# Performance work log

Measured on AMD Instinct MI355X. Metric: run time of the kernel, lower is better.

## Reference

```python
import jax, jax.numpy as jnp
import numpy as np

HEAD_SIZE = 128


def setup_inputs() -> dict:
    key = jax.random.key(0)
    k0, k1, k2, k3 = jax.random.split(key, 4)
    B, S, E, H = 4, 4096, 1024, HEAD_SIZE
    x = jax.random.normal(k0, (B, S, E), dtype=jnp.float32)
    scale = 1.0 / np.sqrt(E).astype(np.float32)
    Wq = jax.random.normal(k1, (E, H), dtype=jnp.float32) * scale
    Wk = jax.random.normal(k2, (E, H), dtype=jnp.float32) * scale
    Wv = jax.random.normal(k3, (E, H), dtype=jnp.float32) * scale
    k_mask = jnp.ones((B, S), dtype=jnp.int32)
    return {"x": x, "Wq": Wq, "Wk": Wk, "Wv": Wv, "k_mask": k_mask}


def reference(x, Wq, Wk, Wv, k_mask):
    # Self-attention path (kv=None), causal=True
    Q = x @ Wq  # [B, S, H]
    K = x @ Wk  # [B, S, H]
    V = x @ Wv  # [B, S, H]
    inv_sqrt_h = np.float32(1.0 / np.sqrt(HEAD_SIZE))
    att = jnp.einsum('bqh,bkh->bqk', Q, K) * inv_sqrt_h  # [B, S, S]
    neg_inf = jnp.float32(-jnp.inf)
    # padding mask over keys: [B, 1, S_k]
    att = jnp.where(k_mask[:, None, :] == 0, neg_inf, att)
    # causal mask: tril over (q_len, k_len)
    S = Q.shape[1]
    c_mask = jnp.tril(jnp.ones((S, S), dtype=bool))  # [S, S]
    att = jnp.where(c_mask[None, :, :], att, neg_inf)
    att = jax.nn.softmax(att, axis=-1)
    return att @ V  # [B, S, H]
```

## Files before the change

### kernel.cpp

```cpp
#include <hip/hip_runtime.h>
#include <hip/hip_bf16.h>

typedef unsigned short u16;
typedef __attribute__((ext_vector_type(8))) short bf16x8;
typedef __attribute__((ext_vector_type(4))) float f32x4;
typedef __attribute__((ext_vector_type(4))) unsigned short u16x4;

#define SQ 4096
#define HQ 128
#define NCHUNK 80

__device__ __forceinline__ u16 f2b(float f) {
  unsigned int u = __float_as_uint(f);
  unsigned int r = (u + 0x7fffu + ((u >> 16) & 1u)) >> 16;
  return (u16)r;
}

__device__ __forceinline__ u16 f2b_fast(float f) {
  __hip_bfloat16 h = __float2bfloat16(f);
  return __builtin_bit_cast(u16, h);
}

__device__ __forceinline__ void gload_lds16(const u16* gsrc, u16* ldst) {
  __builtin_amdgcn_global_load_lds((const __attribute__((address_space(1))) void*)gsrc,
                                   (__attribute__((address_space(3))) void*)ldst, 16, 0, 0);
}

__global__ __launch_bounds__(256) void k_wt(const float* __restrict__ Wq, const float* __restrict__ Wk,
                                            const float* __restrict__ Wv, u16* __restrict__ wt) {
  int idx = blockIdx.x * 256 + threadIdx.x;
  int z = idx >> 17, r = idx & 131071, n = r >> 10, k = r & 1023;
  const float* W = (z == 0) ? Wq : (z == 1) ? Wk : Wv;
  wt[idx] = f2b(W[k * 128 + n]);
}

__global__ __launch_bounds__(512, 4) void k_proj(const float* __restrict__ x, const u16* __restrict__ wt,
                                                 u16* __restrict__ qb, u16* __restrict__ kb,
                                                 u16* __restrict__ vt) {
  int blk = blockIdx.x;
  int t = threadIdx.x;
  int w = t >> 6, lane = t & 63;
  int wm = w >> 2, wn = w & 3;
  int lr = lane & 15, lg = lane >> 4;

  __shared__ __align__(16) u16 xl[2][64 * 32];
  __shared__ __align__(16) u16 wl[2][384 * 32];

  int srow = t >> 3, sc8 = t & 7;
  const float* xg = x + (long)(blk * 64 + srow) * 1024 + sc8 * 4;
  int xch = ((sc8 >> 1) ^ ((srow >> 1) & 3));
  int xoff = srow * 32 + xch * 8 + (sc8 & 1) * 4;

  f32x4 acc[2][6];
#pragma unroll
  for (int i = 0; i < 2; ++i)
#pragma unroll
    for (int j = 0; j < 6; ++j) acc[i][j] = (f32x4){0.f, 0.f, 0.f, 0.f};

  auto stage_w = [&](int bufi, int k0) {
#pragma unroll
    for (int i = 0; i < 3; ++i) {
      int ci = i * 512 + t;
      int row = ci >> 2, ch = ci & 3;
      gload_lds16(wt + (long)row * 1024 + k0 + ((ch ^ ((row >> 1) & 3)) << 3),
                  &wl[bufi][0] + ci * 8);
    }
  };

  {
    float4 xa = *(const float4*)(xg);
    stage_w(0, 0);
    u16x4 o;
    o[0] = f2b(xa.x); o[1] = f2b(xa.y); o[2] = f2b(xa.z); o[3] = f2b(xa.w);
    *(u16x4*)(&xl[0][0] + xoff) = o;
  }
  __syncthreads();

  int arow0 = wm * 32 + lr;
  for (int ks = 0; ks < 32; ++ks) {
    int cur = ks & 1;
    float4 xa;
    bool more = (ks + 1 < 32);
    if (more) {
      xa = *(const float4*)(xg + (ks + 1) * 32);
      stage_w(cur ^ 1, (ks + 1) * 32);
    }
    bf16x8 af[2], bf[6];
#pragma unroll
    for (int i = 0; i < 2; ++i) {
      int row = arow0 + i * 16;
      af[i] = *(const bf16x8*)(&xl[cur][0] + row * 32 + ((lg ^ ((row >> 1) & 3)) << 3));
    }
#pragma unroll
    for (int j = 0; j < 6; ++j) {
      int row = wn * 96 + j * 16 + lr;
      bf[j] = *(const bf16x8*)(&wl[cur][0] + row * 32 + ((lg ^ ((row >> 1) & 3)) << 3));
    }
#pragma unroll
    for (int i = 0; i < 2; ++i)
#pragma unroll
      for (int j = 0; j < 6; ++j)
        acc[i][j] = __builtin_amdgcn_mfma_f32_16x16x32_bf16(af[i], bf[j], acc[i][j], 0, 0, 0);
    if (more) {
      u16x4 o;
      o[0] = f2b(xa.x); o[1] = f2b(xa.y); o[2] = f2b(xa.z); o[3] = f2b(xa.w);
      *(u16x4*)(&xl[cur ^ 1][0] + xoff) = o;
    }
    __syncthreads();
  }

#pragma unroll
  for (int i = 0; i < 2; ++i)
#pragma unroll
    for (int j = 0; j < 6; ++j)
#pragma unroll
      for (int r = 0; r < 4; ++r) {
        int m = blk * 64 + wm * 32 + i * 16 + lg * 4 + r;
        int col = wn * 96 + j * 16 + lr;
        int z = col >> 7, cz = col & 127;
        u16 v = f2b(acc[i][j][r]);
        if (z == 0) qb[(long)m * 128 + cz] = v;
        else if (z == 1) kb[(long)m * 128 + cz] = v;
        else { int bb = m >> 12, sR = m & 4095; vt[(long)bb * 524288 + (long)cz * 4096 + sR] = v; }
      }
}

__global__ __launch_bounds__(512, 4) void k_attn(const u16* __restrict__ qb, const u16* __restrict__ kb,
                                                 const u16* __restrict__ vt, const int* __restrict__ kmask,
                                                 float* __restrict__ po, float* __restrict__ pl) {
  const float SCALE_LOG2 = 0.08838834764831845f * 1.4426950408889634f;
  const float MFIX = 24.0f;
  int f = (NCHUNK - 1) - (int)blockIdx.x;
  int b = blockIdx.y;
  int gg = 0;
  while (gg < 3 && f >= 4 * (gg + 1) * (gg + 2)) ++gg;
  int off = f - 4 * gg * (gg + 1);
  int qt2 = 8 * gg + off / (gg + 1);
  int kc = off - (off / (gg + 1)) * (gg + 1);
  int kt0 = kc * 16;
  int kt1 = min(kt0 + 16, 2 * qt2 + 2);

  int t = threadIdx.x, w = t >> 6, lane = t & 63;
  int lr = lane & 15, lg = lane >> 4, sw = lr & 7;
  int qrow0 = qt2 * 128 + w * 16;
  const u16* Q = qb + ((long)(b * SQ + qrow0)) * HQ;
  const u16* K = kb + (long)b * SQ * HQ;
  const u16* V = vt + (long)b * HQ * SQ;
  const int* msk = kmask + b * SQ;

  __shared__ __align__(16) u16 Kl[2][64 * 128];
  __shared__ __align__(16) u16 Vl[2][128 * 64];
  __shared__ __align__(16) u16 plds[8][16 * 64];

  bf16x8 aq[4];
#pragma unroll
  for (int c = 0; c < 4; ++c) aq[c] = *(const bf16x8*)(Q + lr * HQ + c * 32 + lg * 8);

  bf16x8 ones;
#pragma unroll
  for (int e = 0; e < 8; ++e) ones[e] = (short)0x3F80;

  f32x4 o[8];
#pragma unroll
  for (int n = 0; n < 8; ++n) o[n] = (f32x4){0.f, 0.f, 0.f, 0.f};
  f32x4 l_acc = (f32x4){0.f, 0.f, 0.f, 0.f};

  auto stage = [&](int bufi, int kb0) {
    const u16* Kg = K + (long)kb0 * HQ;
    const u16* Vg = V + kb0;
#pragma unroll
    for (int i = 0; i < 2; ++i) {
      int ci = w * 2 + i;
      int o16 = ci * 64 + lane;
      int row = o16 >> 4, ch = o16 & 15;
      gload_lds16(Kg + row * HQ + ((ch ^ (row & 7)) << 3), &Kl[bufi][ci * 512]);
    }
#pragma unroll
    for (int i = 0; i < 2; ++i) {
      int ci = 16 + w * 2 + i;
      int o16 = (ci - 16) * 64 + lane;
      int row = o16 >> 3, ch = o16 & 7;
      gload_lds16(Vg + (long)row * SQ + ((ch ^ (row & 7)) << 3), &Vl[bufi][(ci - 16) * 512]);
    }
  };

  stage(0, kt0 * 64);
  __syncthreads();

  u16* pw = &plds[w][0];
  for (int kt = kt0; kt < kt1; ++kt) {
    int cur = (kt - kt0) & 1;
    int kb0 = kt * 64;
    if (kt + 1 < kt1) stage(cur ^ 1, kb0 + 64);

    if (kb0 <= qrow0 + 15) {
      f32x4 s[4];
#pragma unroll
      for (int h = 0; h < 4; ++h) {
        f32x4 acc = (f32x4){0.f, 0.f, 0.f, 0.f};
        const u16* Kp = &Kl[cur][(h * 16 + lr) * 128];
#pragma unroll
        for (int c = 0; c < 4; ++c) {
          bf16x8 bk = *(const bf16x8*)(Kp + (((c * 4 + lg) ^ sw) << 3));
          acc = __builtin_amdgcn_mfma_f32_16x16x32_bf16(aq[c], bk, acc, 0, 0, 0);
        }
        s[h] = acc;
      }
      float mf[4];
#pragma unroll
      for (int h = 0; h < 4; ++h) mf[h] = (msk[kb0 + h * 16 + lr] != 0) ? 1.0f : 0.0f;
      bool needc = (kb0 + 63 > qrow0);
#pragma unroll
      for (int r = 0; r < 4; ++r) {
        int row = lg * 4 + r;
        int qr = qrow0 + row;
#pragma unroll
        for (int h = 0; h < 4; ++h) {
          float p = __builtin_exp2f(fmaf(s[h][r], SCALE_LOG2, -MFIX)) * mf[h];
          if (needc) p = ((kb0 + h * 16 + lr) <= qr) ? p : 0.0f;
          int poff = row * 64 + ((((h * 2 + (lr >> 3)) ^ (row & 7))) << 3) + (lr & 7);
          pw[poff] = f2b_fast(p);
        }
      }
      bf16x8 ap0 = *(const bf16x8*)(pw + lr * 64 + ((lg ^ sw) << 3));
      bf16x8 ap1 = *(const bf16x8*)(pw + lr * 64 + (((4 + lg) ^ sw) << 3));
      l_acc = __builtin_amdgcn_mfma_f32_16x16x32_bf16(ap0, ones, l_acc, 0, 0, 0);
      l_acc = __builtin_amdgcn_mfma_f32_16x16x32_bf16(ap1, ones, l_acc, 0, 0, 0);
#pragma unroll
      for (int n = 0; n < 8; ++n) {
        const u16* Vp = &Vl[cur][(n * 16 + lr) * 64];
        bf16x8 bv0 = *(const bf16x8*)(Vp + ((lg ^ sw) << 3));
        bf16x8 bv1 = *(const bf16x8*)(Vp + (((4 + lg) ^ sw) << 3));
        o[n] = __builtin_amdgcn_mfma_f32_16x16x32_bf16(ap0, bv0, o[n], 0, 0, 0);
        o[n] = __builtin_amdgcn_mfma_f32_16x16x32_bf16(ap1, bv1, o[n], 0, 0, 0);
      }
    }
    __syncthreads();
  }

  long p = (long)b * NCHUNK + f;
  float* pob = po + p * 16384;
#pragma unroll
  for (int n = 0; n < 8; ++n)
#pragma unroll
    for (int r = 0; r < 4; ++r)
      pob[(w * 16 + lg * 4 + r) * 128 + n * 16 + lr] = o[n][r];
  if (lr == 0) {
#pragma unroll
    for (int r = 0; r < 4; ++r) pl[p * 128 + w * 16 + lg * 4 + r] = l_acc[r];
  }
}

__global__ __launch_bounds__(256) void k_merge(const float* __restrict__ po, const float* __restrict__ pl,
                                               float* __restrict__ out) {
  int qt2 = blockIdx.x, b = blockIdx.y;
  int gg = qt2 >> 3;
  int nch = gg + 1;
  long pbase = (long)b * NCHUNK + 4 * gg * (gg + 1) + (qt2 & 7) * (gg + 1);
  int t = threadIdx.x;
  int row = t >> 1, c0 = (t & 1) * 64;
  float l = 0.f;
  for (int i = 0; i < nch; ++i) l += pl[(pbase + i) * 128 + row];
  float inv = 1.0f / l;
  const float* p0 = po + pbase * 16384 + row * 128 + c0;
  float* orow = out + ((long)(b * SQ + qt2 * 128 + row)) * HQ + c0;
#pragma unroll
  for (int j = 0; j < 64; j += 4) {
    float4 acc = {0.f, 0.f, 0.f, 0.f};
    for (int i = 0; i < nch; ++i) {
      float4 v = *(const float4*)(p0 + (long)i * 16384 + j);
      acc.x += v.x; acc.y += v.y; acc.z += v.z; acc.w += v.w;
    }
    acc.x *= inv; acc.y *= inv; acc.z *= inv; acc.w *= inv;
    *(float4*)(orow + j) = acc;
  }
}

extern "C" void kernel_launch(void* const* d_in, const int* in_sizes, int n_in,
                              void* d_out, int out_size, void* d_ws, size_t ws_size,
                              hipStream_t stream) {
  const float* x  = (const float*)d_in[0];
  const float* Wq = (const float*)d_in[1];
  const float* Wk = (const float*)d_in[2];
  const float* Wv = (const float*)d_in[3];
  const int* kmask = (const int*)d_in[4];
  char* ws = (char*)d_ws;
  u16* wt = (u16*)(ws + 33554432);
  u16* qb = (u16*)(ws + 34340864);
  u16* kb = (u16*)(ws + 38535168);
  u16* vt = (u16*)(ws + 42729472);
  float* po = (float*)ws;
  float* pl = (float*)(ws + 33554432);
  float* out = (float*)d_out;

  k_wt<<<1536, 256, 0, stream>>>(Wq, Wk, Wv, wt);
  k_proj<<<256, 512, 0, stream>>>(x, wt, qb, kb, vt);
  k_attn<<<dim3(NCHUNK, 4), 512, 0, stream>>>(qb, kb, vt, kmask, po, pl);
  k_merge<<<dim3(32, 4), 256, 0, stream>>>(po, pl, out);
}
```

Measured before the change: 127.3 us.

## Split attention into finer key chunks, store bf16 partials, shrink projection blocks

The attention work split changes from 16-tile key chunks in a grouped layout to 8-tile chunks per 128-row query tile, raising the chunk count from 80 to 144 per batch. The aim is better load balance and more blocks across the GPU's compute units for the causal triangle. Partial attention outputs are now written as bf16 instead of fp32, which halves write and merge read traffic at some accuracy cost. The projection kernel now uses 256-thread blocks over 32 rows, doubling the grid to 512 blocks.

```diff
diff --git a/kernel.cpp b/kernel.cpp
--- a/kernel.cpp
+++ b/kernel.cpp
@@ -8,7 +8,7 @@
 
 #define SQ 4096
 #define HQ 128
-#define NCHUNK 80
+#define NCHUNK 144
 
 __device__ __forceinline__ u16 f2b(float f) {
   unsigned int u = __float_as_uint(f);
@@ -19,6 +19,11 @@
 __device__ __forceinline__ u16 f2b_fast(float f) {
   __hip_bfloat16 h = __float2bfloat16(f);
   return __builtin_bit_cast(u16, h);
+}
+
+__device__ __forceinline__ float b2f(u16 v) {
+  unsigned int u = ((unsigned int)v) << 16;
+  return __uint_as_float(u);
 }
 
 __device__ __forceinline__ void gload_lds16(const u16* gsrc, u16* ldst) {
@@ -34,20 +39,19 @@
   wt[idx] = f2b(W[k * 128 + n]);
 }
 
-__global__ __launch_bounds__(512, 4) void k_proj(const float* __restrict__ x, const u16* __restrict__ wt,
+__global__ __launch_bounds__(256, 3) void k_proj(const float* __restrict__ x, const u16* __restrict__ wt,
                                                  u16* __restrict__ qb, u16* __restrict__ kb,
                                                  u16* __restrict__ vt) {
   int blk = blockIdx.x;
   int t = threadIdx.x;
-  int w = t >> 6, lane = t & 63;
-  int wm = w >> 2, wn = w & 3;
+  int wn = t >> 6, lane = t & 63;
   int lr = lane & 15, lg = lane >> 4;
 
-  __shared__ __align__(16) u16 xl[2][64 * 32];
+  __shared__ __align__(16) u16 xl[2][32 * 32];
   __shared__ __align__(16) u16 wl[2][384 * 32];
 
   int srow = t >> 3, sc8 = t & 7;
-  const float* xg = x + (long)(blk * 64 + srow) * 1024 + sc8 * 4;
+  const float* xg = x + (long)(blk * 32 + srow) * 1024 + sc8 * 4;
   int xch = ((sc8 >> 1) ^ ((srow >> 1) & 3));
   int xoff = srow * 32 + xch * 8 + (sc8 & 1) * 4;
 
@@ -59,8 +63,8 @@
 
   auto stage_w = [&](int bufi, int k0) {
 #pragma unroll
-    for (int i = 0; i < 3; ++i) {
-      int ci = i * 512 + t;
+    for (int i = 0; i < 6; ++i) {
+      int ci = i * 256 + t;
       int row = ci >> 2, ch = ci & 3;
       gload_lds16(wt + (long)row * 1024 + k0 + ((ch ^ ((row >> 1) & 3)) << 3),
                   &wl[bufi][0] + ci * 8);
@@ -76,7 +80,6 @@
   }
   __syncthreads();
 
-  int arow0 = wm * 32 + lr;
   for (int ks = 0; ks < 32; ++ks) {
     int cur = ks & 1;
     float4 xa;
@@ -88,7 +91,7 @@
     bf16x8 af[2], bf[6];
 #pragma unroll
     for (int i = 0; i < 2; ++i) {
-      int row = arow0 + i * 16;
+      int row = i * 16 + lr;
       af[i] = *(const bf16x8*)(&xl[cur][0] + row * 32 + ((lg ^ ((row >> 1) & 3)) << 3));
     }
 #pragma unroll
@@ -115,7 +118,7 @@
     for (int j = 0; j < 6; ++j)
 #pragma unroll
       for (int r = 0; r < 4; ++r) {
-        int m = blk * 64 + wm * 32 + i * 16 + lg * 4 + r;
+        int m = blk * 32 + i * 16 + lg * 4 + r;
         int col = wn * 96 + j * 16 + lr;
         int z = col >> 7, cz = col & 127;
         u16 v = f2b(acc[i][j][r]);
@@ -127,18 +130,17 @@
 
 __global__ __launch_bounds__(512, 4) void k_attn(const u16* __restrict__ qb, const u16* __restrict__ kb,
                                                  const u16* __restrict__ vt, const int* __restrict__ kmask,
-                                                 float* __restrict__ po, float* __restrict__ pl) {
+                                                 u16* __restrict__ po, float* __restrict__ pl) {
   const float SCALE_LOG2 = 0.08838834764831845f * 1.4426950408889634f;
   const float MFIX = 24.0f;
   int f = (NCHUNK - 1) - (int)blockIdx.x;
   int b = blockIdx.y;
-  int gg = 0;
-  while (gg < 3 && f >= 4 * (gg + 1) * (gg + 2)) ++gg;
-  int off = f - 4 * gg * (gg + 1);
-  int qt2 = 8 * gg + off / (gg + 1);
-  int kc = off - (off / (gg + 1)) * (gg + 1);
-  int kt0 = kc * 16;
-  int kt1 = min(kt0 + 16, 2 * qt2 + 2);
+  int qt2 = 0, cum = 0;
+  while (cum + ((qt2 + 4) >> 2) <= f) { cum += (qt2 + 4) >> 2; ++qt2; }
+  int kc = f - cum;
+  int ntile = 2 * qt2 + 2;
+  int kt0 = kc * 8;
+  int kt1 = min(kt0 + 8, ntile);
 
   int t = threadIdx.x, w = t >> 6, lane = t & 63;
   int lr = lane & 15, lg = lane >> 4, sw = lr & 7;
@@ -177,10 +179,10 @@
     }
 #pragma unroll
     for (int i = 0; i < 2; ++i) {
-      int ci = 16 + w * 2 + i;
-      int o16 = (ci - 16) * 64 + lane;
+      int ci = w * 2 + i;
+      int o16 = ci * 64 + lane;
       int row = o16 >> 3, ch = o16 & 7;
-      gload_lds16(Vg + (long)row * SQ + ((ch ^ (row & 7)) << 3), &Vl[bufi][(ci - 16) * 512]);
+      gload_lds16(Vg + (long)row * SQ + ((ch ^ (row & 7)) << 3), &Vl[bufi][ci * 512]);
     }
   };
 
@@ -239,40 +241,41 @@
   }
 
   long p = (long)b * NCHUNK + f;
-  float* pob = po + p * 16384;
+  u16* pob = po + p * 16384;
 #pragma unroll
   for (int n = 0; n < 8; ++n)
 #pragma unroll
     for (int r = 0; r < 4; ++r)
-      pob[(w * 16 + lg * 4 + r) * 128 + n * 16 + lr] = o[n][r];
+      pob[(w * 16 + lg * 4 + r) * 128 + n * 16 + lr] = f2b_fast(o[n][r]);
   if (lr == 0) {
 #pragma unroll
     for (int r = 0; r < 4; ++r) pl[p * 128 + w * 16 + lg * 4 + r] = l_acc[r];
   }
 }
 
-__global__ __launch_bounds__(256) void k_merge(const float* __restrict__ po, const float* __restrict__ pl,
+__global__ __launch_bounds__(256) void k_merge(const u16* __restrict__ po, const float* __restrict__ pl,
                                                float* __restrict__ out) {
   int qt2 = blockIdx.x, b = blockIdx.y;
-  int gg = qt2 >> 3;
-  int nch = gg + 1;
-  long pbase = (long)b * NCHUNK + 4 * gg * (gg + 1) + (qt2 & 7) * (gg + 1);
+  int nch = (qt2 + 4) >> 2;
+  int pre = 0;
+  for (int q = 0; q < qt2; ++q) pre += (q + 4) >> 2;
+  long pbase = (long)b * NCHUNK + pre;
   int t = threadIdx.x;
   int row = t >> 1, c0 = (t & 1) * 64;
   float l = 0.f;
   for (int i = 0; i < nch; ++i) l += pl[(pbase + i) * 128 + row];
   float inv = 1.0f / l;
-  const float* p0 = po + pbase * 16384 + row * 128 + c0;
+  const u16* p0 = po + pbase * 16384 + row * 128 + c0;
   float* orow = out + ((long)(b * SQ + qt2 * 128 + row)) * HQ + c0;
 #pragma unroll
   for (int j = 0; j < 64; j += 4) {
-    float4 acc = {0.f, 0.f, 0.f, 0.f};
+    float acc0 = 0.f, acc1 = 0.f, acc2 = 0.f, acc3 = 0.f;
     for (int i = 0; i < nch; ++i) {
-      float4 v = *(const float4*)(p0 + (long)i * 16384 + j);
-      acc.x += v.x; acc.y += v.y; acc.z += v.z; acc.w += v.w;
-    }
-    acc.x *= inv; acc.y *= inv; acc.z *= inv; acc.w *= inv;
-    *(float4*)(orow + j) = acc;
+      u16x4 v = *(const u16x4*)(p0 + (long)i * 16384 + j);
+      acc0 += b2f(v[0]); acc1 += b2f(v[1]); acc2 += b2f(v[2]); acc3 += b2f(v[3]);
+    }
+    float4 r = {acc0 * inv, acc1 * inv, acc2 * inv, acc3 * inv};
+    *(float4*)(orow + j) = r;
   }
 }
 
@@ -289,12 +292,12 @@
   u16* qb = (u16*)(ws + 34340864);
   u16* kb = (u16*)(ws + 38535168);
   u16* vt = (u16*)(ws + 42729472);
-  float* po = (float*)ws;
+  u16* po = (u16*)ws;
   float* pl = (float*)(ws + 33554432);
   float* out = (float*)d_out;
 
   k_wt<<<1536, 256, 0, stream>>>(Wq, Wk, Wv, wt);
-  k_proj<<<256, 512, 0, stream>>>(x, wt, qb, kb, vt);
+  k_proj<<<512, 256, 0, stream>>>(x, wt, qb, kb, vt);
   k_attn<<<dim3(NCHUNK, 4), 512, 0, stream>>>(qb, kb, vt, kmask, po, pl);
   k_merge<<<dim3(32, 4), 256, 0, stream>>>(po, pl, out);
 }
```

New measurement: 136.1 us. 1.07x slower.
